# Performance work log

Measured on AMD Instinct MI355X. Metric: run time of the kernel, lower is better.

Reference implementation:

```python
import jax, jax.numpy as jnp
import numpy as np

# config constants (match init_kwargs)
SF = 4
H_THRESH = 0.1
HM_SCALE = 3.5
NUM_KP = 32
REGION = 3          # entropy_layer region_size
BANDWIDTH = 0.1     # entropy_layer bandwidth
NUM_BINS = 16       # soft-histogram bins for KDE entropy
W_ME = 100.0
W_CE = 100.0
W_IT = 1.0
MOVE_W = 0.1
BETA = 1.5
KAPPA = 1.0
STATUS_W = 2.5
OVERLAP_W = 10.0
EPS = 1e-10


def _box_mean(x, r):
    # x: (..., H, W) -> rxr box average with SAME padding
    lead = x.shape[:-2]
    flat = x.reshape((-1, 1) + x.shape[-2:])
    k = jnp.ones((1, 1, r, r), x.dtype) / (r * r)
    y = jax.lax.conv_general_dilated(flat, k, (1, 1), 'SAME')
    return y.reshape(lead + x.shape[-2:])


def _local_entropy(images):
    # images: (B, SF, C, H, W) in [0,1]; differentiable local (region_size) KDE entropy,
    # soft histogram with NUM_BINS Gaussian kernels of width BANDWIDTH, averaged over channels.
    bins = jnp.linspace(0.0, 1.0, NUM_BINS).astype(images.dtype)
    k = jnp.exp(-0.5 * ((images[..., None] - bins) / BANDWIDTH) ** 2)  # (B,SF,C,H,W,Nb)
    k = jnp.moveaxis(k, -1, -3)                                        # (B,SF,C,Nb,H,W)
    p = _box_mean(k, REGION)
    p = p / (p.sum(axis=-3, keepdims=True) + EPS)
    ent = -(p * jnp.log(p + EPS)).sum(axis=-3)                          # (B,SF,C,H,W)
    return ent.mean(axis=2)                                             # (B,SF,H,W)


def reference(coords, gaussians, active_status, images):
    N, KP, _ = coords.shape
    _, _, HH, WW = gaussians.shape
    _, C, H, W = images.shape
    images = jax.image.resize(images, (N, C, HH, WW), method='bilinear')
    B = N // SF
    coords = coords.reshape(B, SF, KP, 2)
    active_status = active_status.reshape(B, SF, KP)
    gaussians = gaussians.reshape(B, SF, KP, HH, WW)
    images = images.reshape(B, SF, C, HH, WW)

    heatmaps = jnp.clip(HM_SCALE * jax.nn.relu(gaussians - H_THRESH), 0.0, 1.0)
    heatmap_size = heatmaps[0, 0, 0].sum()

    rgb_entropy = _local_entropy(images)                 # (B,SF,HH,WW)
    shifted_entropy = jnp.roll(rgb_entropy, 1, axis=1)
    joint_entropy = jnp.maximum(rgb_entropy, shifted_entropy)
    cond_entropy = joint_entropy - shifted_entropy
    re_sum = rgb_entropy.sum(axis=(-1, -2))              # (B,SF)
    ce_sum = cond_entropy.sum(axis=(-1, -2))

    active_hm = active_status[..., None, None] * heatmaps          # (B,SF,KP,HH,WW)
    agg_mask = jnp.clip(active_hm.sum(axis=2), 0.0, 1.0)            # (B,SF,HH,WW)
    # (E - E*mask).sum == (E*(1-mask)).sum
    mel = (rgb_entropy * (1.0 - agg_mask)).sum(axis=(-1, -2)) / (re_sum + EPS)
    mcel = (cond_entropy * (1.0 - agg_mask)).sum(axis=(-1, -2)) / (ce_sum + EPS)
    mcel = mcel.at[:, 0].set(0.0)

    shifted_coords = jnp.roll(coords, 1, axis=1)
    dist = jnp.linalg.norm(coords - shifted_coords, axis=-1)        # (B,SF,KP)
    shifted_status = jnp.roll(active_status, 1, axis=1)
    movement_cost = (dist * active_status * shifted_status).sum(axis=-1)  # (B,SF)

    shifted_hm = jnp.roll(active_hm, 1, axis=1)
    se = shifted_entropy[:, :, None]
    re = rgb_entropy[:, :, None]
    ce = cond_entropy[:, :, None]
    source_info = se * (1.0 - active_hm) * (1.0 - shifted_hm)
    target_info = re * active_hm + KAPPA * ce * (1.0 - active_hm)
    recon = source_info + target_info
    mi = recon + re - jnp.maximum(recon, re)
    mi_sum = mi.sum(axis=(-1, -2))                                   # (B,SF,KP)
    sum_current = re_sum[:, :, None]                                 # (B,SF,1)
    reconstruction_cost = ((sum_current - mi_sum) / heatmap_size).mean(axis=-1)  # (B,SF)
    itl = reconstruction_cost + MOVE_W * movement_cost

    status_loss = active_status.sum(axis=-1) / KP
    agg_gauss = gaussians.sum(axis=2)
    overlap = jax.nn.relu(jnp.max(agg_gauss, axis=(-1, -2)) - BETA) / NUM_KP

    mint = (W_ME * mel + W_CE * mcel + W_IT * itl + OVERLAP_W * overlap
            + (1.0 - mel) * STATUS_W * status_loss)
    return mint.mean(axis=-1).mean()


def setup_inputs() -> dict:
    key = jax.random.key(0)
    k1, k2, k3, k4 = jax.random.split(key, 4)
    N, KP, HH, WW, C, H, W = 64, 32, 96, 96, 3, 128, 128
    coords = jax.random.uniform(k1, (N, KP, 2), jnp.float32) * 96.0
    gaussians = jax.random.uniform(k2, (N, KP, HH, WW), jnp.float32)
    active_status = jax.random.uniform(k3, (N, KP), jnp.float32)
    images = jax.random.uniform(k4, (N, C, H, W), jnp.float32)
    return {"coords": coords, "gaussians": gaussians, "active_status": active_status, "images": images}
```

## Files before the change

kernel.cpp:

```cpp
#include <hip/hip_runtime.h>

#define EPSF 1e-10f
#define KPN 32
#define HH 96
#define WW 96
#define NPIX (HH*WW)
#define CH 3
#define SH 128
#define SW 128
#define NIMG 64

__device__ inline float wred_sum(float v){
  #pragma unroll
  for(int off=32; off; off>>=1) v += __shfl_xor(v, off, 64);
  return v;
}
__device__ inline float wred_max(float v){
  #pragma unroll
  for(int off=32; off; off>>=1) v = fmaxf(v, __shfl_xor(v, off, 64));
  return v;
}

__global__ __launch_bounds__(256) void k_resize(const float* __restrict__ img, float* __restrict__ out){
  int idx = blockIdx.x*256 + threadIdx.x;
  if (idx >= NIMG*CH*NPIX) return;
  int ox = idx % WW;
  int oy = (idx / WW) % HH;
  int nc = idx / NPIX;
  float xs = (ox + 0.5f)*(4.0f/3.0f) - 0.5f;
  float ys = (oy + 0.5f)*(4.0f/3.0f) - 0.5f;
  int jx0 = (int)ceilf(xs - 4.0f/3.0f);
  int jy0 = (int)ceilf(ys - 4.0f/3.0f);
  float wx[3], wy[3]; float sx=0.f, sy=0.f;
  #pragma unroll
  for(int t=0;t<3;t++){
    int j = jx0+t;
    float w = 1.0f - 0.75f*fabsf((float)j - xs);
    w = (j>=0 && j<SW) ? fmaxf(w,0.0f) : 0.0f;
    wx[t]=w; sx+=w;
    j = jy0+t;
    w = 1.0f - 0.75f*fabsf((float)j - ys);
    w = (j>=0 && j<SH) ? fmaxf(w,0.0f) : 0.0f;
    wy[t]=w; sy+=w;
  }
  float inv = 1.0f/(sx*sy);
  const float* base = img + (size_t)nc*SH*SW;
  float acc=0.f;
  #pragma unroll
  for(int ty=0;ty<3;ty++){
    if (wy[ty]==0.f) continue;
    int jy = min(max(jy0+ty,0), SH-1);
    #pragma unroll
    for(int tx=0;tx<3;tx++){
      if (wx[tx]==0.f) continue;
      int jx = min(max(jx0+tx,0), SW-1);
      acc += wy[ty]*wx[tx]*base[jy*SW+jx];
    }
  }
  out[idx] = acc*inv;
}

__global__ __launch_bounds__(256, 2) void k_entropy(const float* __restrict__ rimg, float* __restrict__ entC){
  int tid = threadIdx.x;
  int n = blockIdx.y;
  int ch = blockIdx.z;
  int wave = tid >> 6, lane = tid & 63;
  int half = lane >> 5, cl = lane & 31;
  int rp = wave*2 + half;
  int r0 = blockIdx.x*16 + rp*2;
  int c0 = cl*3;
  const float* src = rimg + ((size_t)(n*CH+ch))*NPIX;
  float v[4][3];
  #pragma unroll
  for (int r=0;r<4;r++){
    int gr = r0-1+r;
    bool rok = (gr>=0 && gr<HH);
    #pragma unroll
    for (int c=0;c<3;c++){
      v[r][c] = rok ? src[gr*96 + c0 + c] : 1e4f;
    }
  }
  float S[2][3]={{0,0,0},{0,0,0}}, T[2][3]={{0,0,0},{0,0,0}};
  #pragma unroll
  for (int b=0;b<16;b++){
    float cb = (float)b * (1.0f/15.0f);
    float k[4][3];
    #pragma unroll
    for (int r=0;r<4;r++)
      #pragma unroll
      for (int c=0;c<3;c++){
        float d = v[r][c] - cb;
        k[r][c] = __expf(-50.f*d*d);
      }
    #pragma unroll
    for (int o=0;o<2;o++){
      float cs0 = k[o][0]+k[o+1][0]+k[o+2][0];
      float cs1 = k[o][1]+k[o+1][1]+k[o+2][1];
      float cs2 = k[o][2]+k[o+1][2]+k[o+2][2];
      float lf = __shfl_up(cs2, 1, 64);  if (cl==0)  lf = 0.f;
      float rt = __shfl_down(cs0, 1, 64); if (cl==31) rt = 0.f;
      float p0 = (lf +cs0+cs1)*(1.f/9.f);
      float p1 = (cs0+cs1+cs2)*(1.f/9.f);
      float p2 = (cs1+cs2+rt )*(1.f/9.f);
      S[o][0]+=p0; T[o][0]+=p0*__logf(p0+EPSF);
      S[o][1]+=p1; T[o][1]+=p1*__logf(p1+EPSF);
      S[o][2]+=p2; T[o][2]+=p2*__logf(p2+EPSF);
    }
  }
  float* dst = entC + ((size_t)(ch*NIMG + n))*NPIX;
  #pragma unroll
  for (int o=0;o<2;o++)
    #pragma unroll
    for (int j=0;j<3;j++){
      float Sp = S[o][j]+EPSF;
      float e = (__logf(Sp) - T[o][j]/Sp)*(1.f/3.f);
      dst[(size_t)(r0+o)*96 + (c0+j)] = e;
    }
}

__global__ __launch_bounds__(256, 4) void k_main(const float* __restrict__ gauss,
                                              const float* __restrict__ status,
                                              const float* __restrict__ entC,
                                              float* __restrict__ miS,
                                              float* __restrict__ melN,
                                              float* __restrict__ mcelN,
                                              float* __restrict__ reS,
                                              float* __restrict__ ceS,
                                              unsigned int* __restrict__ gmax,
                                              float* __restrict__ hsG){
  __shared__ float stc[32], stq[32];
  int tid = threadIdx.x;
  int lane = tid & 63;
  int wgid = blockIdx.x;
  int xcd = wgid & 7;
  int q_ = wgid >> 3;
  int tile = q_ % 9;
  int n = xcd*8 + q_/9;
  int s = n & 3;
  int np = (s==0) ? n+3 : n-1;
  bool nz = (n==0);
  if (tid < 32) stc[tid] = status[n*32 + tid];
  else if (tid < 64) stq[tid-32] = status[np*32 + (tid-32)];
  __syncthreads();
  unsigned off = (unsigned)(tile*256 + tid);
  const float4* __restrict__ gc = (const float4*)gauss + (size_t)n*32*2304 + off;
  const float4* __restrict__ gq = (const float4*)gauss + (size_t)np*32*2304 + off;
  const float4* __restrict__ ec = (const float4*)entC;
  float4 e0 = ec[(size_t)(0*NIMG + n)*2304 + off];
  float4 e1 = ec[(size_t)(1*NIMG + n)*2304 + off];
  float4 e2c = ec[(size_t)(2*NIMG + n)*2304 + off];
  float4 f0 = ec[(size_t)(0*NIMG + np)*2304 + off];
  float4 f1 = ec[(size_t)(1*NIMG + np)*2304 + off];
  float4 f2 = ec[(size_t)(2*NIMG + np)*2304 + off];
  float4 re2, se2;
  re2.x = e0.x+e1.x+e2c.x; re2.y = e0.y+e1.y+e2c.y; re2.z = e0.z+e1.z+e2c.z; re2.w = e0.w+e1.w+e2c.w;
  se2.x = f0.x+f1.x+f2.x;  se2.y = f0.y+f1.y+f2.y;  se2.z = f0.z+f1.z+f2.z;  se2.w = f0.w+f1.w+f2.w;
  float4 ce, K2;
  ce.x = fmaxf(re2.x, se2.x) - se2.x;  K2.x = fmaxf(se2.x - re2.x, 0.f);
  ce.y = fmaxf(re2.y, se2.y) - se2.y;  K2.y = fmaxf(se2.y - re2.y, 0.f);
  ce.z = fmaxf(re2.z, se2.z) - se2.z;  K2.z = fmaxf(se2.z - re2.z, 0.f);
  ce.w = fmaxf(re2.w, se2.w) - se2.w;  K2.w = fmaxf(se2.w - re2.w, 0.f);
  float4 am = make_float4(0,0,0,0), ag = make_float4(0,0,0,0), mi = make_float4(0,0,0,0);
  float hsacc = 0.f;
  float4 G[8], H[8];

#define GLD(dst, addr) asm volatile("global_load_dwordx4 %0, %1, off" : "=v"(dst) : "v"(addr) : "memory")
#define VMWAIT(N) asm volatile("s_waitcnt vmcnt(" #N ")" ::: "memory")

#define PC(g, h, CMP, sc, sp) { \
  float hm = fminf(fmaxf(__builtin_fmaf((g).CMP, 3.5f, -0.35f), 0.f), 1.f); \
  float hp = fminf(fmaxf(__builtin_fmaf((h).CMP, 3.5f, -0.35f), 0.f), 1.f); \
  hsl += hm; \
  float ah = (sc)*hm, sh = (sp)*hp; \
  am.CMP += ah; ag.CMP += (g).CMP; \
  float D = __builtin_fmaf(-se2.CMP, sh, K2.CMP); \
  mi.CMP += fminf((1.f - ah)*D, 0.f); }

#define PROC(g, h, KP) { \
  float sc = stc[KP], sp = stq[KP]; \
  float hsl = 0.f; \
  PC(g, h, x, sc, sp) PC(g, h, y, sc, sp) PC(g, h, z, sc, sp) PC(g, h, w, sc, sp) \
  if (nz && (KP)==0) hsacc = hsl; }

#define STEP(I, WN) { \
  VMWAIT(WN); \
  __builtin_amdgcn_sched_barrier(0); \
  PROC(G[(I)&7], H[(I)&7], (I)); \
  if ((I) < 24){ GLD(G[(I)&7], gc + ((I)+8)*2304); GLD(H[(I)&7], gq + ((I)+8)*2304); } \
}

  __builtin_amdgcn_sched_barrier(0);
  #pragma unroll
  for (int j=0;j<8;j++){ GLD(G[j], gc + j*2304); GLD(H[j], gq + j*2304); }

  STEP(0,14)  STEP(1,14)  STEP(2,14)  STEP(3,14)
  STEP(4,14)  STEP(5,14)  STEP(6,14)  STEP(7,14)
  STEP(8,14)  STEP(9,14)  STEP(10,14) STEP(11,14)
  STEP(12,14) STEP(13,14) STEP(14,14) STEP(15,14)
  STEP(16,14) STEP(17,14) STEP(18,14) STEP(19,14)
  STEP(20,14) STEP(21,14) STEP(22,14) STEP(23,14)
  STEP(24,14) STEP(25,12) STEP(26,10) STEP(27,8)
  STEP(28,6)  STEP(29,4)  STEP(30,2)  STEP(31,0)

#undef STEP
#undef PROC
#undef PC
#undef VMWAIT
#undef GLD

  float qx = 1.f - fminf(am.x, 1.f);
  float qy = 1.f - fminf(am.y, 1.f);
  float qz = 1.f - fminf(am.z, 1.f);
  float qw = 1.f - fminf(am.w, 1.f);
  float r1 = wred_sum(re2.x*qx + re2.y*qy + re2.z*qz + re2.w*qw);
  float r2 = wred_sum(ce.x*qx + ce.y*qy + ce.z*qz + ce.w*qw);
  float r3 = wred_sum(re2.x + re2.y + re2.z + re2.w);
  float r4 = wred_sum(ce.x + ce.y + ce.z + ce.w);
  float r5 = wred_max(fmaxf(fmaxf(ag.x, ag.y), fmaxf(ag.z, ag.w)));
  float r6 = wred_sum(mi.x + mi.y + mi.z + mi.w);
  if (lane==0){
    atomicAdd(&melN[n], r1);
    atomicAdd(&mcelN[n], r2);
    atomicAdd(&reS[n], r3);
    atomicAdd(&ceS[n], r4);
    atomicMax(&gmax[n], __float_as_uint(r5));
    atomicAdd(&miS[n], r6);
  }
  if (nz){
    float h = wred_sum(hsacc);
    if (lane==0) atomicAdd(hsG, h);
  }
}

__global__ __launch_bounds__(256) void k_final(const float* __restrict__ coords,
                                               const float* __restrict__ status,
                                               const float* __restrict__ miS,
                                               const float* __restrict__ melN,
                                               const float* __restrict__ mcelN,
                                               const float* __restrict__ reS,
                                               const float* __restrict__ ceS,
                                               const unsigned int* __restrict__ gmax,
                                               const float* __restrict__ hsG,
                                               float* __restrict__ out){
  __shared__ float wsum[4];
  int tid = threadIdx.x;
  int n = tid >> 2, q = tid & 3;
  int s = n & 3;
  int np = (s==0) ? n+3 : n-1;
  float mc = 0.f, sl = 0.f;
  #pragma unroll
  for (int j=0;j<8;j++){
    int kp = q*8 + j;
    float dx = coords[(n*KPN+kp)*2+0] - coords[(np*KPN+kp)*2+0];
    float dy = coords[(n*KPN+kp)*2+1] - coords[(np*KPN+kp)*2+1];
    float st = status[n*KPN+kp];
    mc += sqrtf(dx*dx+dy*dy) * st * status[np*KPN+kp];
    sl += st;
  }
  mc += __shfl_xor(mc,1,64); mc += __shfl_xor(mc,2,64);
  sl += __shfl_xor(sl,1,64); sl += __shfl_xor(sl,2,64);
  float mint = 0.f;
  if (q==0){
    sl *= (1.f/KPN);
    float rsum = reS[n];
    float mel = melN[n]/(rsum+EPSF);
    float mcel = (s==0) ? 0.f : mcelN[n]/(ceS[n]+EPSF);
    float rc = (-miS[n]*(1.f/KPN)) / hsG[0];
    float itl = rc + 0.1f*mc;
    float ovl = fmaxf(__uint_as_float(gmax[n]) - 1.5f, 0.f)*(1.f/KPN);
    mint = 100.f*mel + 100.f*mcel + itl + 10.f*ovl + (1.f-mel)*2.5f*sl;
  }
  float r = wred_sum(mint);
  if ((tid&63)==0) wsum[tid>>6] = r;
  __syncthreads();
  if (tid==0) out[0] = (wsum[0]+wsum[1]+wsum[2]+wsum[3])*(1.f/64.f);
}

extern "C" void kernel_launch(void* const* d_in, const int* in_sizes, int n_in,
                              void* d_out, int out_size, void* d_ws, size_t ws_size,
                              hipStream_t stream){
  const float* coords = (const float*)d_in[0];
  const float* gauss  = (const float*)d_in[1];
  const float* status = (const float*)d_in[2];
  const float* images = (const float*)d_in[3];
  float* out = (float*)d_out;
  float* rimg = (float*)d_ws;
  float* entC = rimg + (size_t)NIMG*CH*NPIX;
  float* miS  = entC + (size_t)CH*NIMG*NPIX;
  float* melN = miS + 64;
  float* mcelN = melN + 64;
  float* reS   = mcelN + 64;
  float* ceS   = reS + 64;
  unsigned int* gmax = (unsigned int*)(ceS + 64);
  float* hsG = (float*)(gmax + 64);
  hipMemsetAsync(miS, 0, (6*64 + 1)*sizeof(float), stream);
  k_resize<<<(NIMG*CH*NPIX + 255)/256, 256, 0, stream>>>(images, rimg);
  k_entropy<<<dim3(6,64,3), 256, 0, stream>>>(rimg, entC);
  k_main<<<576, 256, 0, stream>>>(gauss, status, entC, miS, melN, mcelN, reS, ceS, gmax, hsG);
  k_final<<<1,256,0,stream>>>(coords, status, miS, melN, mcelN, reS, ceS, gmax, hsG, out);
}
```

Measured before the change: 84.05 us.

## Split entropy bins across two thread halves and expand Gaussian exponent algebraically

The entropy kernel now runs 512 threads per block. Each half handles 8 of the 16 histogram bins, and the halves combine their partial S/T sums through shared memory. The Gaussian kernel exponent is expanded into a per-pixel quadratic plus a per-bin constant, so each term becomes one FMA, an add and exp2f instead of a subtract, square, multiply and exp. The goal is to double thread-level parallelism for the exp/log-heavy loop and to trim the ALU ops per term, at the cost of a block barrier and LDS traffic. The expanded exponent also carries more rounding error, since it subtracts large terms that nearly cancel.

```diff
diff --git a/kernel.cpp b/kernel.cpp
--- a/kernel.cpp
+++ b/kernel.cpp
@@ -60,38 +60,45 @@
   out[idx] = acc*inv;
 }
 
-__global__ __launch_bounds__(256, 2) void k_entropy(const float* __restrict__ rimg, float* __restrict__ entC){
+__global__ __launch_bounds__(512) void k_entropy(const float* __restrict__ rimg, float* __restrict__ entC){
+  __shared__ float SP[6][256], TP[6][256];
   int tid = threadIdx.x;
+  int hb = tid >> 8;
+  int l = tid & 255;
   int n = blockIdx.y;
   int ch = blockIdx.z;
-  int wave = tid >> 6, lane = tid & 63;
+  int wave = l >> 6, lane = l & 63;
   int half = lane >> 5, cl = lane & 31;
   int rp = wave*2 + half;
   int r0 = blockIdx.x*16 + rp*2;
   int c0 = cl*3;
   const float* src = rimg + ((size_t)(n*CH+ch))*NPIX;
-  float v[4][3];
+  const float L2E = 1.4426950408889634f;
+  const float GAM = -50.f*L2E/225.f;
+  float a[4][3], be[4][3];
   #pragma unroll
   for (int r=0;r<4;r++){
     int gr = r0-1+r;
     bool rok = (gr>=0 && gr<HH);
     #pragma unroll
     for (int c=0;c<3;c++){
-      v[r][c] = rok ? src[gr*96 + c0 + c] : 1e4f;
+      float v = rok ? src[gr*96 + c0 + c] : 1e4f;
+      a[r][c]  = -50.f*L2E*v*v;
+      be[r][c] = (100.f/15.f)*L2E*v;
     }
   }
   float S[2][3]={{0,0,0},{0,0,0}}, T[2][3]={{0,0,0},{0,0,0}};
-  #pragma unroll
-  for (int b=0;b<16;b++){
-    float cb = (float)b * (1.0f/15.0f);
+  float bf0 = (float)(hb*8);
+  #pragma unroll
+  for (int b=0;b<8;b++){
+    float bf = bf0 + (float)b;
+    float cc = GAM*bf*bf;
     float k[4][3];
     #pragma unroll
     for (int r=0;r<4;r++)
       #pragma unroll
-      for (int c=0;c<3;c++){
-        float d = v[r][c] - cb;
-        k[r][c] = __expf(-50.f*d*d);
-      }
+      for (int c=0;c<3;c++)
+        k[r][c] = exp2f(__builtin_fmaf(be[r][c], bf, a[r][c]) + cc);
     #pragma unroll
     for (int o=0;o<2;o++){
       float cs0 = k[o][0]+k[o+1][0]+k[o+2][0];
@@ -107,15 +114,29 @@
       S[o][2]+=p2; T[o][2]+=p2*__logf(p2+EPSF);
     }
   }
-  float* dst = entC + ((size_t)(ch*NIMG + n))*NPIX;
-  #pragma unroll
-  for (int o=0;o<2;o++)
-    #pragma unroll
-    for (int j=0;j<3;j++){
-      float Sp = S[o][j]+EPSF;
-      float e = (__logf(Sp) - T[o][j]/Sp)*(1.f/3.f);
-      dst[(size_t)(r0+o)*96 + (c0+j)] = e;
-    }
+  if (hb==1){
+    #pragma unroll
+    for (int o=0;o<2;o++)
+      #pragma unroll
+      for (int j=0;j<3;j++){
+        SP[o*3+j][l] = S[o][j];
+        TP[o*3+j][l] = T[o][j];
+      }
+  }
+  __syncthreads();
+  if (hb==0){
+    float* dst = entC + ((size_t)(ch*NIMG + n))*NPIX;
+    #pragma unroll
+    for (int o=0;o<2;o++)
+      #pragma unroll
+      for (int j=0;j<3;j++){
+        int i = o*3+j;
+        float Ss = S[o][j] + SP[i][l];
+        float Tt = T[o][j] + TP[i][l];
+        float Sp = Ss+EPSF;
+        dst[(size_t)(r0+o)*96 + (c0+j)] = (__logf(Sp) - Tt/Sp)*(1.f/3.f);
+      }
+  }
 }
 
 __global__ __launch_bounds__(256, 4) void k_main(const float* __restrict__ gauss,
@@ -295,7 +316,7 @@
   float* hsG = (float*)(gmax + 64);
   hipMemsetAsync(miS, 0, (6*64 + 1)*sizeof(float), stream);
   k_resize<<<(NIMG*CH*NPIX + 255)/256, 256, 0, stream>>>(images, rimg);
-  k_entropy<<<dim3(6,64,3), 256, 0, stream>>>(rimg, entC);
+  k_entropy<<<dim3(6,64,3), 512, 0, stream>>>(rimg, entC);
   k_main<<<576, 256, 0, stream>>>(gauss, status, entC, miS, melN, mcelN, reS, ceS, gmax, hsG);
   k_final<<<1,256,0,stream>>>(coords, status, miS, melN, mcelN, reS, ceS, gmax, hsG, out);
 }
```

Result: slower. 87.68 us (+4.3%).
